# Kernel tuning notes

Hardware: AMD Instinct MI355X
Metric: run time of the kernel (lower is better)

The kernel has to match this reference:

```python
import math
import jax, jax.numpy as jnp
import numpy as np

D_MODEL = 1024
N_HEADS = 16
HEAD_DIM = D_MODEL // N_HEADS
B, L = 1, 4096


def _slopes(n_heads):
    ratio = 2.0 ** (-8.0 / n_heads)
    return jnp.asarray([ratio ** (i + 1) for i in range(n_heads)], dtype=jnp.float32)


def setup_inputs() -> dict:
    key = jax.random.key(0)
    ks = jax.random.split(key, 5)
    scale = 1.0 / math.sqrt(D_MODEL)
    return {
        "x": jax.random.normal(ks[0], (B, L, D_MODEL), dtype=jnp.float32),
        "q_w": jax.random.normal(ks[1], (D_MODEL, D_MODEL), dtype=jnp.float32) * scale,
        "k_w": jax.random.normal(ks[2], (D_MODEL, D_MODEL), dtype=jnp.float32) * scale,
        "v_w": jax.random.normal(ks[3], (D_MODEL, D_MODEL), dtype=jnp.float32) * scale,
        "o_w": jax.random.normal(ks[4], (D_MODEL, D_MODEL), dtype=jnp.float32) * scale,
    }


def reference(x, q_w, k_w, v_w, o_w):
    b, l, _ = x.shape
    # projections -> [B, H, L, hd]
    def proj(w):
        return (x @ w).reshape(b, l, N_HEADS, HEAD_DIM).transpose(0, 2, 1, 3)
    q, k, v = proj(q_w), proj(k_w), proj(v_w)

    scale = math.sqrt(HEAD_DIM)
    scores = jnp.einsum("bhid,bhjd->bhij", q, k) / scale  # [B,H,L,L]

    pos = jnp.arange(l)
    distance = jnp.abs(pos[None, :] - pos[:, None]).astype(jnp.float32)  # [L,L]
    alibi = -distance[None, :, :] * _slopes(N_HEADS)[:, None, None]       # [H,L,L]
    scores = scores + alibi[None]

    causal = pos[None, :] <= pos[:, None]  # j <= i
    scores = jnp.where(causal[None, None], scores, -jnp.inf)

    attn = jax.nn.softmax(scores, axis=-1)
    out = jnp.einsum("bhij,bhjd->bhid", attn, v)
    out = out.transpose(0, 2, 1, 3).reshape(b, l, D_MODEL)
    return out @ o_w
```

## Files before the change

kernel.cpp:

```cpp
#include <hip/hip_runtime.h>

#define L_SEQ 4096
#define DM    1024
#define NH    16
#define HD    64

typedef unsigned short ushort_t;
typedef __attribute__((ext_vector_type(8))) short bf16x8;
typedef __attribute__((ext_vector_type(4))) float f32x4;

__device__ inline unsigned short f2bf(float f) {
    union { float f; unsigned int u; } v; v.f = f;
    unsigned int r = v.u + 0x7fffu + ((v.u >> 16) & 1u);
    return (unsigned short)(r >> 16);
}

__device__ inline unsigned cvt_pk_bf16(float lo, float hi) {
    unsigned w;
    asm("v_cvt_pk_bf16_f32 %0, %1, %2" : "=v"(w) : "v"(lo), "v"(hi));
    return w;
}

__device__ inline float ex2(float x) {
#if __has_builtin(__builtin_amdgcn_exp2f)
    return __builtin_amdgcn_exp2f(x);
#else
    return exp2f(x);
#endif
}

__device__ inline void load_lds16(const ushort_t* g, ushort_t* l) {
    __builtin_amdgcn_global_load_lds(
        (const __attribute__((address_space(1))) unsigned int*)g,
        (__attribute__((address_space(3))) unsigned int*)l, 16, 0, 0);
}

__device__ inline bool detect_f32(const ushort_t* xraw) {
    __shared__ int s_flag;
    const int t = threadIdx.x;
    if (t < 64) {
        unsigned e = (xraw[2 * t] >> 7) & 0xFFu;
        unsigned long long m = __ballot(e >= 0x88u);
        if (t == 0) s_flag = (__popcll(m) >= 8) ? 1 : 0;
    }
    __syncthreads();
    return s_flag != 0;
}

__global__ __launch_bounds__(256) void convert_all(const void* __restrict__ xv,
                                                   const void* __restrict__ w0,
                                                   const void* __restrict__ w1,
                                                   const void* __restrict__ w2,
                                                   const void* __restrict__ w3,
                                                   ushort_t* __restrict__ xb,
                                                   ushort_t* __restrict__ wT) {
    bool f32 = detect_f32((const ushort_t*)xv);
    const int z = blockIdx.z;
    const int t = threadIdx.x;

    if (z == 4) {
        const int B0 = (blockIdx.y * 16 + blockIdx.x) * 16384;
        #pragma unroll
        for (int it = 0; it < 8; ++it) {
            const int i = B0 + it * 2048 + t * 8;
            if (f32) {
                const float* xf = (const float*)xv;
                float4 v0 = *(const float4*)(xf + i);
                float4 v1 = *(const float4*)(xf + i + 4);
                uint4 u;
                u.x = cvt_pk_bf16(v0.x, v0.y);
                u.y = cvt_pk_bf16(v0.z, v0.w);
                u.z = cvt_pk_bf16(v1.x, v1.y);
                u.w = cvt_pk_bf16(v1.z, v1.w);
                *(uint4*)(xb + i) = u;
            } else {
                *(uint4*)(xb + i) = *(const uint4*)((const ushort_t*)xv + i);
            }
        }
        return;
    }

    const void* w = (z == 0) ? w0 : (z == 1) ? w1 : (z == 2) ? w2 : w3;
    ushort_t* out = wT + (size_t)z * (DM * DM);
    __shared__ ushort_t T[64][65];
    const int k0 = blockIdx.x * 64, n0 = blockIdx.y * 64;
    #pragma unroll
    for (int i = 0; i < 16; ++i) {
        int e = t + i * 256;
        int r = e >> 6, c = e & 63;
        T[r][c] = f32 ? f2bf(((const float*)w)[(size_t)(k0 + r) * DM + n0 + c])
                      : ((const ushort_t*)w)[(size_t)(k0 + r) * DM + n0 + c];
    }
    __syncthreads();
    #pragma unroll
    for (int i = 0; i < 16; ++i) {
        int e = t + i * 256;
        int d = e >> 6, l = e & 63;
        out[(size_t)(n0 + d) * DM + k0 + l] = T[l][d];
    }
}

__device__ inline void gemm128_body(const ushort_t* __restrict__ A,
                                    const ushort_t* __restrict__ Bt,
                                    void* __restrict__ Cv, int cmode,
                                    int m0, int n0) {
    constexpr int K = 1024, NOUT = 1024;
    __shared__ ushort_t As[128 * 64];
    __shared__ ushort_t Bs[128 * 64];

    const int t = threadIdx.x, lane = t & 63, wave = t >> 6;
    const int l15 = lane & 15, quad = lane >> 4;
    const int mw = (wave >> 1) * 64, nw = (wave & 1) * 64;
    const int srow = lane >> 3;
    const int sgr  = (lane & 7) ^ (lane >> 3);
    const int swz  = l15 & 7;

    f32x4 acc[4][4] = {};

    for (int k0 = 0; k0 < K; k0 += 64) {
        #pragma unroll
        for (int i = 0; i < 4; ++i) {
            const int j = wave * 4 + i;
            load_lds16(A  + (size_t)(m0 + 8 * j + srow) * K + k0 + sgr * 8,
                       &As[8 * j * 64]);
            load_lds16(Bt + (size_t)(n0 + 8 * j + srow) * K + k0 + sgr * 8,
                       &Bs[8 * j * 64]);
        }
        __syncthreads();

        #pragma unroll
        for (int kt = 0; kt < 2; ++kt) {
            bf16x8 af[4], bf[4];
            #pragma unroll
            for (int i = 0; i < 4; ++i) {
                af[i] = *(const bf16x8*)&As[(mw + i * 16 + l15) * 64
                                            + (((kt * 4 + quad) ^ swz) * 8)];
                bf[i] = *(const bf16x8*)&Bs[(nw + i * 16 + l15) * 64
                                            + (((kt * 4 + quad) ^ swz) * 8)];
            }
            #pragma unroll
            for (int mt = 0; mt < 4; ++mt)
                #pragma unroll
                for (int nt = 0; nt < 4; ++nt)
                    acc[mt][nt] = __builtin_amdgcn_mfma_f32_16x16x32_bf16(
                        af[mt], bf[nt], acc[mt][nt], 0, 0, 0);
        }
        __syncthreads();
    }

    if (cmode == 2) {
        ushort_t* Vt = (ushort_t*)Cv;
        #pragma unroll
        for (int mt = 0; mt < 4; ++mt)
            #pragma unroll
            for (int nt = 0; nt < 4; ++nt) {
                int col  = n0 + nw + nt * 16 + l15;
                int row0 = m0 + mw + mt * 16 + quad * 4;
                ushort_t pk[4] = {f2bf(acc[mt][nt][0]), f2bf(acc[mt][nt][1]),
                                  f2bf(acc[mt][nt][2]), f2bf(acc[mt][nt][3])};
                *(uint2*)&Vt[(size_t)col * L_SEQ + row0] = *(const uint2*)pk;
            }
        return;
    }

    const int odd = lane & 1;
    #pragma unroll
    for (int mtp = 0; mtp < 2; ++mtp)
        #pragma unroll
        for (int nt = 0; nt < 4; ++nt)
            #pragma unroll
            for (int r = 0; r < 4; ++r) {
                float zA = acc[2 * mtp][nt][r];
                float zB = acc[2 * mtp + 1][nt][r];
                float send = odd ? zA : zB;
                float got  = __shfl_xor(send, 1);
                const int row = m0 + mw + (2 * mtp + odd) * 16 + quad * 4 + r;
                const int col = n0 + nw + nt * 16 + (l15 & ~1);
                if (cmode == 1) {
                    float2 w2 = odd ? make_float2(got, zB) : make_float2(zA, got);
                    *(float2*)((float*)Cv + (size_t)row * NOUT + col) = w2;
                } else {
                    float lo = odd ? got : zA;
                    float hi = odd ? zB  : got;
                    unsigned w = cvt_pk_bf16(lo, hi);
                    *(unsigned*)((ushort_t*)Cv + (size_t)row * NOUT + col) = w;
                }
            }
}

__global__ __launch_bounds__(256) void qkv128(const ushort_t* __restrict__ xb,
                                              const ushort_t* __restrict__ wT,
                                              ushort_t* Qp, ushort_t* Kp, ushort_t* Vt) {
    const int b = blockIdx.x;
    const int n0 = (b & 7) * 128;
    const int u  = b >> 3;
    const int m0 = (u / 3) * 128;
    const int z  = u % 3;
    const ushort_t* Bt = wT + (size_t)z * (DM * DM);
    if (z == 0)      gemm128_body(xb, Bt, Qp, 0, m0, n0);
    else if (z == 1) gemm128_body(xb, Bt, Kp, 0, m0, n0);
    else             gemm128_body(xb, Bt, Vt, 2, m0, n0);
}

__global__ __launch_bounds__(256) void ogemm128(const void* __restrict__ xdet,
                                                const ushort_t* __restrict__ An,
                                                const ushort_t* __restrict__ woT,
                                                void* __restrict__ C) {
    bool f32 = detect_f32((const ushort_t*)xdet);
    const int b = blockIdx.x;
    const int n0 = (b & 7) * 128, m0 = (b >> 3) * 128;
    gemm128_body(An, woT, C, f32 ? 1 : 0, m0, n0);
}

__global__ __launch_bounds__(512) void attn_kernel(const ushort_t* __restrict__ Q,
                                                   const ushort_t* __restrict__ Kp,
                                                   const ushort_t* __restrict__ Vt,
                                                   ushort_t* __restrict__ O) {
    __shared__ ushort_t Ks[2][128 * 64];
    __shared__ ushort_t Vs[2][64 * 128];
    __shared__ ushort_t Pt[128 * 128];

    const int b    = blockIdx.x;
    const int h    = 2 * (b & 7) + ((b >> 3) & 1);
    const int px   = b >> 4;
    const int t    = threadIdx.x;
    const int lane = t & 63, wave = t >> 6;
    const int l15  = lane & 15, quad = lane >> 4;
    const float LOG2E  = 1.44269504f;
    const float slope2 = exp2f(-0.5f * (float)(h + 1)) * LOG2E;
    const float c0     = 0.125f * LOG2E;
    const float qd4f   = (float)(quad * 4);

    const int krow = lane >> 3, kgr = (lane & 7) ^ (lane >> 3);
    const int vsub = lane >> 4;
    const int swz = l15 & 7;

    auto stage_load = [&](int buf, int kv0) {
        #pragma unroll
        for (int i = 0; i < 2; ++i) {
            const int j = wave * 2 + i;
            load_lds16(Kp + (size_t)(kv0 + 8 * j + krow) * DM + h * HD + kgr * 8,
                       &Ks[buf][8 * j * 64]);
        }
        #pragma unroll
        for (int i = 0; i < 2; ++i) {
            const int j = wave * 2 + i;
            const int d = 4 * j + vsub;
            const int g = (lane & 15) ^ (4 * (j & 1) + vsub);
            load_lds16(Vt + (size_t)(h * HD + d) * L_SEQ + kv0 + g * 8,
                       &Vs[buf][4 * j * 128]);
        }
    };

    int par = 0;
    stage_load(0, 0);

    #pragma unroll
    for (int half = 0; half < 2; ++half) {
        const int qb = half ? px : (31 - px);
        const int q0 = qb * 128;
        const int qg = q0 + wave * 16 + l15;
        const float qf = (float)qg;
        const int nst = half ? (px + 1) : (32 - px);

        bf16x8 bq[2];
        #pragma unroll
        for (int kt = 0; kt < 2; ++kt)
            bq[kt] = *(const bf16x8*)(Q + (size_t)qg * DM + h * HD + kt * 32 + quad * 8);

        f32x4 acc_o[4] = {};
        float l_r = 0.f;

        for (int s = 0; s < nst; ++s) {
            const int kv0 = s * 128;
            __syncthreads();

            const int nkv0 = (s + 1 < nst) ? (s + 1) * 128 : 0;
            stage_load(par ^ 1, nkv0);

            f32x4 sacc[8];
            #pragma unroll
            for (int mt = 0; mt < 8; ++mt) sacc[mt] = (f32x4){0.f, 0.f, 0.f, 0.f};
            __builtin_amdgcn_s_setprio(1);
            #pragma unroll
            for (int kt = 0; kt < 2; ++kt)
                #pragma unroll
                for (int mt = 0; mt < 8; ++mt) {
                    bf16x8 a = *(const bf16x8*)&Ks[par][(mt * 16 + l15) * 64
                                                        + (((kt * 4 + quad) ^ swz) * 8)];
                    sacc[mt] = __builtin_amdgcn_mfma_f32_16x16x32_bf16(a, bq[kt], sacc[mt], 0, 0, 0);
                }
            __builtin_amdgcn_s_setprio(0);

            const bool diag = (kv0 + 128 > q0);
            const float off = slope2 * ((float)kv0 + qd4f - qf);
            float rs = 0.f;
            #pragma unroll
            for (int mt = 0; mt < 8; ++mt)
                #pragma unroll
                for (int r = 0; r < 4; ++r) {
                    float kvl = (float)(mt * 16 + r);
                    float s2  = fmaf(sacc[mt][r], c0, fmaf(slope2, kvl, off));
                    if (diag) {
                        int kvg = kv0 + mt * 16 + quad * 4 + r;
                        s2 = (kvg <= qg) ? s2 : -1e30f;
                    }
                    float p = ex2(s2);
                    sacc[mt][r] = p;
                    rs += p;
                }
            rs += __shfl_xor(rs, 16);
            rs += __shfl_xor(rs, 32);
            l_r += rs;

            #pragma unroll
            for (int mt = 0; mt < 8; ++mt) {
                union { float f; unsigned u; } a0, a1, a2, a3;
                a0.f = sacc[mt][0]; a1.f = sacc[mt][1];
                a2.f = sacc[mt][2]; a3.f = sacc[mt][3];
                uint2 w;
                w.x = __builtin_amdgcn_perm(a1.u, a0.u, 0x07060302);
                w.y = __builtin_amdgcn_perm(a3.u, a2.u, 0x07060302);
                const int g = mt * 2 + (quad >> 1);
                *(uint2*)&Pt[(wave * 16 + l15) * 128
                             + ((g ^ swz) * 8 + (quad & 1) * 4)] = w;
            }
            __threadfence_block();

            __builtin_amdgcn_s_setprio(1);
            #pragma unroll
            for (int kt = 0; kt < 4; ++kt) {
                bf16x8 a = *(const bf16x8*)&Pt[(wave * 16 + l15) * 128
                                               + (((kt * 4 + quad) ^ swz) * 8)];
                #pragma unroll
                for (int nt = 0; nt < 4; ++nt) {
                    bf16x8 bvv = *(const bf16x8*)&Vs[par][(nt * 16 + l15) * 128
                                                          + (((kt * 4 + quad) ^ swz) * 8)];
                    acc_o[nt] = __builtin_amdgcn_mfma_f32_16x16x32_bf16(a, bvv, acc_o[nt], 0, 0, 0);
                }
            }
            __builtin_amdgcn_s_setprio(0);

            par ^= 1;
        }

        float linv[4];
        #pragma unroll
        for (int r = 0; r < 4; ++r) linv[r] = 1.0f / __shfl(l_r, quad * 4 + r);
        #pragma unroll
        for (int nt = 0; nt < 4; ++nt)
            #pragma unroll
            for (int r = 0; r < 4; ++r) {
                int row = q0 + wave * 16 + quad * 4 + r;
                O[(size_t)row * DM + h * HD + nt * 16 + l15] = f2bf(acc_o[nt][r] * linv[r]);
            }
    }
}

__global__ __launch_bounds__(512, 4) void attn_split(const ushort_t* __restrict__ Q,
                                                     const ushort_t* __restrict__ Kp,
                                                     const ushort_t* __restrict__ Vt,
                                                     float* __restrict__ Op,
                                                     float* __restrict__ Lp) {
    __shared__ ushort_t Ks[128 * 64];
    __shared__ ushort_t Vs[64 * 128];
    __shared__ ushort_t Pt[128 * 128];

    const int b    = blockIdx.x;
    const int bb   = b & 255;
    const int v    = b >> 8;
    const int h    = 2 * (bb & 7) + ((bb >> 3) & 1);
    const int px   = bb >> 4;
    const int t    = threadIdx.x;
    const int lane = t & 63, wave = t >> 6;
    const int l15  = lane & 15, quad = lane >> 4;
    const float LOG2E  = 1.44269504f;
    const float slope2 = exp2f(-0.5f * (float)(h + 1)) * LOG2E;
    const float c0     = 0.125f * LOG2E;
    const float qd4f   = (float)(quad * 4);

    const int krow = lane >> 3, kgr = (lane & 7) ^ (lane >> 3);
    const int vsub = lane >> 4;
    const int swz = l15 & 7;

    float* Opv = Op + (size_t)v * L_SEQ * DM;

    auto stage_load = [&](int kv0) {
        #pragma unroll
        for (int i = 0; i < 2; ++i) {
            const int j = wave * 2 + i;
            load_lds16(Kp + (size_t)(kv0 + 8 * j + krow) * DM + h * HD + kgr * 8,
                       &Ks[8 * j * 64]);
        }
        #pragma unroll
        for (int i = 0; i < 2; ++i) {
            const int j = wave * 2 + i;
            const int d = 4 * j + vsub;
            const int g = (lane & 15) ^ (4 * (j & 1) + vsub);
            load_lds16(Vt + (size_t)(h * HD + d) * L_SEQ + kv0 + g * 8,
                       &Vs[4 * j * 128]);
        }
    };

    #pragma unroll
    for (int half = 0; half < 2; ++half) {
        const int qb = half ? px : (31 - px);
        const int q0 = qb * 128;
        const int qg = q0 + wave * 16 + l15;
        const float qf = (float)qg;
        const int nst = half ? (px + 1) : (32 - px);

        bf16x8 bq[2];
        #pragma unroll
        for (int kt = 0; kt < 2; ++kt)
            bq[kt] = *(const bf16x8*)(Q + (size_t)qg * DM + h * HD + kt * 32 + quad * 8);

        f32x4 acc_o[4] = {};
        float l_r = 0.f;

        for (int s = v; s < nst; s += 2) {
            const int kv0 = s * 128;
            stage_load(kv0);
            __syncthreads();

            f32x4 sacc[8];
            #pragma unroll
            for (int mt = 0; mt < 8; ++mt) sacc[mt] = (f32x4){0.f, 0.f, 0.f, 0.f};
            __builtin_amdgcn_s_setprio(1);
            #pragma unroll
            for (int kt = 0; kt < 2; ++kt)
                #pragma unroll
                for (int mt = 0; mt < 8; ++mt) {
                    bf16x8 a = *(const bf16x8*)&Ks[(mt * 16 + l15) * 64
                                                   + (((kt * 4 + quad) ^ swz) * 8)];
                    sacc[mt] = __builtin_amdgcn_mfma_f32_16x16x32_bf16(a, bq[kt], sacc[mt], 0, 0, 0);
                }
            __builtin_amdgcn_s_setprio(0);

            const bool diag = (kv0 + 128 > q0);
            const float off = slope2 * ((float)kv0 + qd4f - qf);
            float rs = 0.f;
            #pragma unroll
            for (int mt = 0; mt < 8; ++mt)
                #pragma unroll
                for (int r = 0; r < 4; ++r) {
                    float kvl = (float)(mt * 16 + r);
                    float s2  = fmaf(sacc[mt][r], c0, fmaf(slope2, kvl, off));
                    if (diag) {
                        int kvg = kv0 + mt * 16 + quad * 4 + r;
                        s2 = (kvg <= qg) ? s2 : -1e30f;
                    }
                    float p = ex2(s2);
                    sacc[mt][r] = p;
                    rs += p;
                }
            rs += __shfl_xor(rs, 16);
            rs += __shfl_xor(rs, 32);
            l_r += rs;

            #pragma unroll
            for (int mt = 0; mt < 8; ++mt) {
                union { float f; unsigned u; } a0, a1, a2, a3;
                a0.f = sacc[mt][0]; a1.f = sacc[mt][1];
                a2.f = sacc[mt][2]; a3.f = sacc[mt][3];
                uint2 w;
                w.x = __builtin_amdgcn_perm(a1.u, a0.u, 0x07060302);
                w.y = __builtin_amdgcn_perm(a3.u, a2.u, 0x07060302);
                const int g = mt * 2 + (quad >> 1);
                *(uint2*)&Pt[(wave * 16 + l15) * 128
                             + ((g ^ swz) * 8 + (quad & 1) * 4)] = w;
            }
            __threadfence_block();

            __builtin_amdgcn_s_setprio(1);
            #pragma unroll
            for (int kt = 0; kt < 4; ++kt) {
                bf16x8 a = *(const bf16x8*)&Pt[(wave * 16 + l15) * 128
                                               + (((kt * 4 + quad) ^ swz) * 8)];
                #pragma unroll
                for (int nt = 0; nt < 4; ++nt) {
                    bf16x8 bvv = *(const bf16x8*)&Vs[(nt * 16 + l15) * 128
                                                     + (((kt * 4 + quad) ^ swz) * 8)];
                    acc_o[nt] = __builtin_amdgcn_mfma_f32_16x16x32_bf16(a, bvv, acc_o[nt], 0, 0, 0);
                }
            }
            __builtin_amdgcn_s_setprio(0);

            __syncthreads();
        }

        #pragma unroll
        for (int nt = 0; nt < 4; ++nt)
            #pragma unroll
            for (int r = 0; r < 4; ++r) {
                int row = q0 + wave * 16 + quad * 4 + r;
                Opv[(size_t)row * DM + h * HD + nt * 16 + l15] = acc_o[nt][r];
            }
        if (quad == 0)
            Lp[(size_t)v * (NH * L_SEQ) + (size_t)h * L_SEQ + qg] = l_r;
    }
}

__global__ __launch_bounds__(256) void attn_combine(const float* __restrict__ Op,
                                                    const float* __restrict__ Lp,
                                                    ushort_t* __restrict__ An) {
    const int i = (blockIdx.x * 256 + threadIdx.x) * 8;
    const int row = i >> 10;
    const int h   = (i & 1023) >> 6;
    const float l0 = Lp[(size_t)h * L_SEQ + row];
    const float l1 = Lp[(size_t)NH * L_SEQ + (size_t)h * L_SEQ + row];
    const float linv = 1.0f / (l0 + l1);
    const size_t V1 = (size_t)L_SEQ * DM;
    float4 a0 = *(const float4*)(Op + i);
    float4 a1 = *(const float4*)(Op + i + 4);
    float4 b0 = *(const float4*)(Op + V1 + i);
    float4 b1 = *(const float4*)(Op + V1 + i + 4);
    uint4 u;
    u.x = cvt_pk_bf16((a0.x + b0.x) * linv, (a0.y + b0.y) * linv);
    u.y = cvt_pk_bf16((a0.z + b0.z) * linv, (a0.w + b0.w) * linv);
    u.z = cvt_pk_bf16((a1.x + b1.x) * linv, (a1.y + b1.y) * linv);
    u.w = cvt_pk_bf16((a1.z + b1.z) * linv, (a1.w + b1.w) * linv);
    *(uint4*)(An + i) = u;
}

__global__ __launch_bounds__(512, 8) void attn_split4(const ushort_t* __restrict__ Q,
                                                      const ushort_t* __restrict__ Kp,
                                                      const ushort_t* __restrict__ Vt,
                                                      float* __restrict__ Op,
                                                      float* __restrict__ Lp) {
    __shared__ ushort_t Ks[64 * 64];
    __shared__ ushort_t Vs[64 * 64];
    __shared__ ushort_t Pt[128 * 64];

    const int b    = blockIdx.x;
    const int bb   = b & 255;
    const int v    = b >> 8;
    const int h    = 2 * (bb & 7) + ((bb >> 3) & 1);
    const int px   = bb >> 4;
    const int t    = threadIdx.x;
    const int lane = t & 63, wave = t >> 6;
    const int l15  = lane & 15, quad = lane >> 4;
    const float LOG2E  = 1.44269504f;
    const float slope2 = exp2f(-0.5f * (float)(h + 1)) * LOG2E;
    const float c0     = 0.125f * LOG2E;
    const float qd4f   = (float)(quad * 4);

    const int krow = lane >> 3, kgr = (lane & 7) ^ (lane >> 3);
    const int swz = l15 & 7;

    float* Opv = Op + (size_t)v * L_SEQ * DM;

    auto stage_load = [&](int kv0) {
        load_lds16(Kp + (size_t)(kv0 + 8 * wave + krow) * DM + h * HD + kgr * 8,
                   &Ks[8 * wave * 64]);
        load_lds16(Vt + (size_t)(h * HD + 8 * wave + krow) * L_SEQ + kv0 + kgr * 8,
                   &Vs[8 * wave * 64]);
    };

    #pragma unroll
    for (int half = 0; half < 2; ++half) {
        const int qb = half ? px : (31 - px);
        const int q0 = qb * 128;
        const int qg = q0 + wave * 16 + l15;
        const float qf = (float)qg;
        const int nst = half ? (2 * px + 2) : (64 - 2 * px);

        bf16x8 bq[2];
        #pragma unroll
        for (int kt = 0; kt < 2; ++kt)
            bq[kt] = *(const bf16x8*)(Q + (size_t)qg * DM + h * HD + kt * 32 + quad * 8);

        f32x4 acc_o[4] = {};
        float l_r = 0.f;

        for (int s = v; s < nst; s += 4) {
            const int kv0 = s * 64;
            stage_load(kv0);
            __syncthreads();

            f32x4 sacc[4];
            #pragma unroll
            for (int mt = 0; mt < 4; ++mt) sacc[mt] = (f32x4){0.f, 0.f, 0.f, 0.f};
            __builtin_amdgcn_s_setprio(1);
            #pragma unroll
            for (int kt = 0; kt < 2; ++kt)
                #pragma unroll
                for (int mt = 0; mt < 4; ++mt) {
                    bf16x8 a = *(const bf16x8*)&Ks[(mt * 16 + l15) * 64
                                                   + (((kt * 4 + quad) ^ swz) * 8)];
                    sacc[mt] = __builtin_amdgcn_mfma_f32_16x16x32_bf16(a, bq[kt], sacc[mt], 0, 0, 0);
                }
            __builtin_amdgcn_s_setprio(0);

            const bool diag = (kv0 + 64 > q0);
            const float off = slope2 * ((float)kv0 + qd4f - qf);
            float rs = 0.f;
            #pragma unroll
            for (int mt = 0; mt < 4; ++mt)
                #pragma unroll
                for (int r = 0; r < 4; ++r) {
                    float kvl = (float)(mt * 16 + r);
                    float s2  = fmaf(sacc[mt][r], c0, fmaf(slope2, kvl, off));
                    if (diag) {
                        int kvg = kv0 + mt * 16 + quad * 4 + r;
                        s2 = (kvg <= qg) ? s2 : -1e30f;
                    }
                    float p = ex2(s2);
                    sacc[mt][r] = p;
                    rs += p;
                }
            rs += __shfl_xor(rs, 16);
            rs += __shfl_xor(rs, 32);
            l_r += rs;

            #pragma unroll
            for (int mt = 0; mt < 4; ++mt) {
                union { float f; unsigned u; } a0, a1, a2, a3;
                a0.f = sacc[mt][0]; a1.f = sacc[mt][1];
                a2.f = sacc[mt][2]; a3.f = sacc[mt][3];
                uint2 w;
                w.x = __builtin_amdgcn_perm(a1.u, a0.u, 0x07060302);
                w.y = __builtin_amdgcn_perm(a3.u, a2.u, 0x07060302);
                const int g = mt * 2 + (quad >> 1);
                *(uint2*)&Pt[(wave * 16 + l15) * 64
                             + ((g ^ swz) * 8 + (quad & 1) * 4)] = w;
            }
            __threadfence_block();

            __builtin_amdgcn_s_setprio(1);
            #pragma unroll
            for (int kt = 0; kt < 2; ++kt) {
                bf16x8 a = *(const bf16x8*)&Pt[(wave * 16 + l15) * 64
                                               + (((kt * 4 + quad) ^ swz) * 8)];
                #pragma unroll
                for (int nt = 0; nt < 4; ++nt) {
                    bf16x8 bvv = *(const bf16x8*)&Vs[(nt * 16 + l15) * 64
                                                     + (((kt * 4 + quad) ^ swz) * 8)];
                    acc_o[nt] = __builtin_amdgcn_mfma_f32_16x16x32_bf16(a, bvv, acc_o[nt], 0, 0, 0);
                }
            }
            __builtin_amdgcn_s_setprio(0);

            __syncthreads();
        }

        #pragma unroll
        for (int nt = 0; nt < 4; ++nt)
            #pragma unroll
            for (int r = 0; r < 4; ++r) {
                int row = q0 + wave * 16 + quad * 4 + r;
                Opv[(size_t)row * DM + h * HD + nt * 16 + l15] = acc_o[nt][r];
            }
        if (quad == 0)
            Lp[(size_t)v * (NH * L_SEQ) + (size_t)h * L_SEQ + qg] = l_r;
    }
}

__global__ __launch_bounds__(256) void attn_combine4(const float* __restrict__ Op,
                                                     const float* __restrict__ Lp,
                                                     ushort_t* __restrict__ An) {
    const int i = (blockIdx.x * 256 + threadIdx.x) * 8;
    const int row = i >> 10;
    const int h   = (i & 1023) >> 6;
    float l = 0.f;
    #pragma unroll
    for (int v = 0; v < 4; ++v)
        l += Lp[(size_t)v * (NH * L_SEQ) + (size_t)h * L_SEQ + row];
    const float linv = 1.0f / l;
    const size_t V1 = (size_t)L_SEQ * DM;
    float4 s0 = {0, 0, 0, 0}, s1 = {0, 0, 0, 0};
    #pragma unroll
    for (int v = 0; v < 4; ++v) {
        float4 a0 = *(const float4*)(Op + (size_t)v * V1 + i);
        float4 a1 = *(const float4*)(Op + (size_t)v * V1 + i + 4);
        s0.x += a0.x; s0.y += a0.y; s0.z += a0.z; s0.w += a0.w;
        s1.x += a1.x; s1.y += a1.y; s1.z += a1.z; s1.w += a1.w;
    }
    uint4 u;
    u.x = cvt_pk_bf16(s0.x * linv, s0.y * linv);
    u.y = cvt_pk_bf16(s0.z * linv, s0.w * linv);
    u.z = cvt_pk_bf16(s1.x * linv, s1.y * linv);
    u.w = cvt_pk_bf16(s1.z * linv, s1.w * linv);
    *(uint4*)(An + i) = u;
}

extern "C" void kernel_launch(void* const* d_in, const int* in_sizes, int n_in,
                              void* d_out, int out_size, void* d_ws, size_t ws_size,
                              hipStream_t stream) {
    const void* x  = d_in[0];
    const void* wq = d_in[1];
    const void* wk = d_in[2];
    const void* wv = d_in[3];
    const void* wo = d_in[4];

    const size_t SZ = (size_t)L_SEQ * DM;
    const size_t WZ = (size_t)DM * DM;
    ushort_t* xb = (ushort_t*)d_ws;
    ushort_t* wT = xb + SZ;
    ushort_t* Qp = wT + 4 * WZ;
    ushort_t* Kp = Qp + SZ;
    ushort_t* Vt = Kp + SZ;
    ushort_t* An = xb;

    float* Op = (float*)(Vt + SZ);
    float* Lp4 = Op + 4 * SZ;
    float* Lp2 = Op + 2 * SZ;
    const size_t base  = 40ull * 1024 * 1024;
    const size_t need4 = base + 4 * SZ * 4 + 4ull * NH * L_SEQ * 4;
    const size_t need2 = base + 2 * SZ * 4 + 2ull * NH * L_SEQ * 4;

    convert_all<<<dim3(16, 16, 5), 256, 0, stream>>>(x, wq, wk, wv, wo, xb, wT);
    qkv128<<<768, 256, 0, stream>>>(xb, wT, Qp, Kp, Vt);
    if (ws_size >= need4) {
        attn_split4<<<1024, 512, 0, stream>>>(Qp, Kp, Vt, Op, Lp4);
        attn_combine4<<<2048, 256, 0, stream>>>(Op, Lp4, An);
    } else if (ws_size >= need2) {
        attn_split<<<512, 512, 0, stream>>>(Qp, Kp, Vt, Op, Lp2);
        attn_combine<<<2048, 256, 0, stream>>>(Op, Lp2, An);
    } else {
        attn_kernel<<<256, 512, 0, stream>>>(Qp, Kp, Vt, An);
    }
    ogemm128<<<256, 256, 0, stream>>>(x, An, wT + 3 * WZ, d_out);
}
```

Baseline: 260.9 us.

## Use 128-wide KV tiles and split attention KV range three ways

The split-KV attention kernel now stages 128 keys per iteration instead of 64 and divides the KV range among 3 blocks per query tile instead of 4. The grid shrinks from 1024 to 768 blocks, and the combine kernel reduces three partials. Larger tiles halve the number of barrier and stage rounds per block, and fewer partials cut the Op/Lp traffic in the combine. In exchange each block uses more LDS and registers (launch bounds drop to 6), and the diagonal masking now covers wider tiles.

```diff
diff --git a/kernel.cpp b/kernel.cpp
--- a/kernel.cpp
+++ b/kernel.cpp
@@ -523,13 +523,13 @@
     *(uint4*)(An + i) = u;
 }
 
-__global__ __launch_bounds__(512, 8) void attn_split4(const ushort_t* __restrict__ Q,
+__global__ __launch_bounds__(512, 6) void attn_split3(const ushort_t* __restrict__ Q,
                                                       const ushort_t* __restrict__ Kp,
                                                       const ushort_t* __restrict__ Vt,
                                                       float* __restrict__ Op,
                                                       float* __restrict__ Lp) {
-    __shared__ ushort_t Ks[64 * 64];
-    __shared__ ushort_t Vs[64 * 64];
+    __shared__ ushort_t Ks[128 * 64];
+    __shared__ ushort_t Vs[64 * 128];
     __shared__ ushort_t Pt[128 * 64];
 
     const int b    = blockIdx.x;
@@ -546,15 +546,26 @@
     const float qd4f   = (float)(quad * 4);
 
     const int krow = lane >> 3, kgr = (lane & 7) ^ (lane >> 3);
+    const int vsub = lane >> 4;
     const int swz = l15 & 7;
 
     float* Opv = Op + (size_t)v * L_SEQ * DM;
 
     auto stage_load = [&](int kv0) {
-        load_lds16(Kp + (size_t)(kv0 + 8 * wave + krow) * DM + h * HD + kgr * 8,
-                   &Ks[8 * wave * 64]);
-        load_lds16(Vt + (size_t)(h * HD + 8 * wave + krow) * L_SEQ + kv0 + kgr * 8,
-                   &Vs[8 * wave * 64]);
+        #pragma unroll
+        for (int i = 0; i < 2; ++i) {
+            const int j = wave * 2 + i;
+            load_lds16(Kp + (size_t)(kv0 + 8 * j + krow) * DM + h * HD + kgr * 8,
+                       &Ks[8 * j * 64]);
+        }
+        #pragma unroll
+        for (int i = 0; i < 2; ++i) {
+            const int j = wave * 2 + i;
+            const int d = 4 * j + vsub;
+            const int g = (lane & 15) ^ (4 * (j & 1) + vsub);
+            load_lds16(Vt + (size_t)(h * HD + d) * L_SEQ + kv0 + g * 8,
+                       &Vs[4 * j * 128]);
+        }
     };
 
     #pragma unroll
@@ -563,7 +574,7 @@
         const int q0 = qb * 128;
         const int qg = q0 + wave * 16 + l15;
         const float qf = (float)qg;
-        const int nst = half ? (2 * px + 2) : (64 - 2 * px);
+        const int nst = half ? (px + 1) : (32 - px);
 
         bf16x8 bq[2];
         #pragma unroll
@@ -573,30 +584,30 @@
         f32x4 acc_o[4] = {};
         float l_r = 0.f;
 
-        for (int s = v; s < nst; s += 4) {
-            const int kv0 = s * 64;
+        for (int s = v; s < nst; s += 3) {
+            const int kv0 = s * 128;
             stage_load(kv0);
             __syncthreads();
 
-            f32x4 sacc[4];
-            #pragma unroll
-            for (int mt = 0; mt < 4; ++mt) sacc[mt] = (f32x4){0.f, 0.f, 0.f, 0.f};
+            f32x4 sacc[8];
+            #pragma unroll
+            for (int mt = 0; mt < 8; ++mt) sacc[mt] = (f32x4){0.f, 0.f, 0.f, 0.f};
             __builtin_amdgcn_s_setprio(1);
             #pragma unroll
             for (int kt = 0; kt < 2; ++kt)
                 #pragma unroll
-                for (int mt = 0; mt < 4; ++mt) {
+                for (int mt = 0; mt < 8; ++mt) {
                     bf16x8 a = *(const bf16x8*)&Ks[(mt * 16 + l15) * 64
                                                    + (((kt * 4 + quad) ^ swz) * 8)];
                     sacc[mt] = __builtin_amdgcn_mfma_f32_16x16x32_bf16(a, bq[kt], sacc[mt], 0, 0, 0);
                 }
             __builtin_amdgcn_s_setprio(0);
 
-            const bool diag = (kv0 + 64 > q0);
+            const bool diag = (kv0 + 128 > q0);
             const float off = slope2 * ((float)kv0 + qd4f - qf);
             float rs = 0.f;
             #pragma unroll
-            for (int mt = 0; mt < 4; ++mt)
+            for (int mt = 0; mt < 8; ++mt)
                 #pragma unroll
                 for (int r = 0; r < 4; ++r) {
                     float kvl = (float)(mt * 16 + r);
@@ -614,32 +625,37 @@
             l_r += rs;
 
             #pragma unroll
-            for (int mt = 0; mt < 4; ++mt) {
-                union { float f; unsigned u; } a0, a1, a2, a3;
-                a0.f = sacc[mt][0]; a1.f = sacc[mt][1];
-                a2.f = sacc[mt][2]; a3.f = sacc[mt][3];
-                uint2 w;
-                w.x = __builtin_amdgcn_perm(a1.u, a0.u, 0x07060302);
-                w.y = __builtin_amdgcn_perm(a3.u, a2.u, 0x07060302);
-                const int g = mt * 2 + (quad >> 1);
-                *(uint2*)&Pt[(wave * 16 + l15) * 64
-                             + ((g ^ swz) * 8 + (quad & 1) * 4)] = w;
-            }
-            __threadfence_block();
-
-            __builtin_amdgcn_s_setprio(1);
-            #pragma unroll
-            for (int kt = 0; kt < 2; ++kt) {
-                bf16x8 a = *(const bf16x8*)&Pt[(wave * 16 + l15) * 64
-                                               + (((kt * 4 + quad) ^ swz) * 8)];
-                #pragma unroll
-                for (int nt = 0; nt < 4; ++nt) {
-                    bf16x8 bvv = *(const bf16x8*)&Vs[(nt * 16 + l15) * 64
-                                                     + (((kt * 4 + quad) ^ swz) * 8)];
-                    acc_o[nt] = __builtin_amdgcn_mfma_f32_16x16x32_bf16(a, bvv, acc_o[nt], 0, 0, 0);
-                }
-            }
-            __builtin_amdgcn_s_setprio(0);
+            for (int h2 = 0; h2 < 2; ++h2) {
+                #pragma unroll
+                for (int mtl = 0; mtl < 4; ++mtl) {
+                    const int mt = h2 * 4 + mtl;
+                    union { float f; unsigned u; } a0, a1, a2, a3;
+                    a0.f = sacc[mt][0]; a1.f = sacc[mt][1];
+                    a2.f = sacc[mt][2]; a3.f = sacc[mt][3];
+                    uint2 w;
+                    w.x = __builtin_amdgcn_perm(a1.u, a0.u, 0x07060302);
+                    w.y = __builtin_amdgcn_perm(a3.u, a2.u, 0x07060302);
+                    const int g = mtl * 2 + (quad >> 1);
+                    *(uint2*)&Pt[(wave * 16 + l15) * 64
+                                 + ((g ^ swz) * 8 + (quad & 1) * 4)] = w;
+                }
+                __threadfence_block();
+
+                __builtin_amdgcn_s_setprio(1);
+                #pragma unroll
+                for (int kt = 0; kt < 2; ++kt) {
+                    bf16x8 a = *(const bf16x8*)&Pt[(wave * 16 + l15) * 64
+                                                   + (((kt * 4 + quad) ^ swz) * 8)];
+                    const int ktg = h2 * 2 + kt;
+                    #pragma unroll
+                    for (int nt = 0; nt < 4; ++nt) {
+                        bf16x8 bvv = *(const bf16x8*)&Vs[(nt * 16 + l15) * 128
+                                                         + (((ktg * 4 + quad) ^ swz) * 8)];
+                        acc_o[nt] = __builtin_amdgcn_mfma_f32_16x16x32_bf16(a, bvv, acc_o[nt], 0, 0, 0);
+                    }
+                }
+                __builtin_amdgcn_s_setprio(0);
+            }
 
             __syncthreads();
         }
@@ -656,7 +672,7 @@
     }
 }
 
-__global__ __launch_bounds__(256) void attn_combine4(const float* __restrict__ Op,
+__global__ __launch_bounds__(256) void attn_combine3(const float* __restrict__ Op,
                                                      const float* __restrict__ Lp,
                                                      ushort_t* __restrict__ An) {
     const int i = (blockIdx.x * 256 + threadIdx.x) * 8;
@@ -664,13 +680,13 @@
     const int h   = (i & 1023) >> 6;
     float l = 0.f;
     #pragma unroll
-    for (int v = 0; v < 4; ++v)
+    for (int v = 0; v < 3; ++v)
         l += Lp[(size_t)v * (NH * L_SEQ) + (size_t)h * L_SEQ + row];
     const float linv = 1.0f / l;
     const size_t V1 = (size_t)L_SEQ * DM;
     float4 s0 = {0, 0, 0, 0}, s1 = {0, 0, 0, 0};
     #pragma unroll
-    for (int v = 0; v < 4; ++v) {
+    for (int v = 0; v < 3; ++v) {
         float4 a0 = *(const float4*)(Op + (size_t)v * V1 + i);
         float4 a1 = *(const float4*)(Op + (size_t)v * V1 + i + 4);
         s0.x += a0.x; s0.y += a0.y; s0.z += a0.z; s0.w += a0.w;
@@ -703,17 +719,17 @@
     ushort_t* An = xb;
 
     float* Op = (float*)(Vt + SZ);
-    float* Lp4 = Op + 4 * SZ;
+    float* Lp3 = Op + 3 * SZ;
     float* Lp2 = Op + 2 * SZ;
     const size_t base  = 40ull * 1024 * 1024;
-    const size_t need4 = base + 4 * SZ * 4 + 4ull * NH * L_SEQ * 4;
+    const size_t need3 = base + 3 * SZ * 4 + 3ull * NH * L_SEQ * 4;
     const size_t need2 = base + 2 * SZ * 4 + 2ull * NH * L_SEQ * 4;
 
     convert_all<<<dim3(16, 16, 5), 256, 0, stream>>>(x, wq, wk, wv, wo, xb, wT);
     qkv128<<<768, 256, 0, stream>>>(xb, wT, Qp, Kp, Vt);
-    if (ws_size >= need4) {
-        attn_split4<<<1024, 512, 0, stream>>>(Qp, Kp, Vt, Op, Lp4);
-        attn_combine4<<<2048, 256, 0, stream>>>(Op, Lp4, An);
+    if (ws_size >= need3) {
+        attn_split3<<<768, 512, 0, stream>>>(Qp, Kp, Vt, Op, Lp3);
+        attn_combine3<<<2048, 256, 0, stream>>>(Op, Lp3, An);
     } else if (ws_size >= need2) {
         attn_split<<<512, 512, 0, stream>>>(Qp, Kp, Vt, Op, Lp2);
         attn_combine<<<2048, 256, 0, stream>>>(Op, Lp2, An);
```

Result: slower. 269.9 us (+3.5%).
